# Performance work log

Measured on AMD Instinct MI355X. Metric: run time of the kernel, lower is better.

Reference implementation:

```python
import jax, jax.numpy as jnp
import numpy as np

N = 20000   # nodes
E = 160000  # edges
G = 32      # graphs in the batch
IN_DIM, HID, OUT = 27, 512, 256


def _linear_init(key, fan_in, fan_out):
    s = 1.0 / np.sqrt(fan_in)
    return jax.random.uniform(key, (fan_in, fan_out), jnp.float32, -s, s)


def setup_inputs() -> dict:
    key = jax.random.key(0)
    ks = jax.random.split(key, 16)
    feature = jax.random.normal(ks[0], (N, IN_DIM), jnp.float32)
    edge_src = jax.random.randint(ks[1], (E,), 0, N, jnp.int32)
    edge_dst = jax.random.randint(ks[2], (E,), 0, N, jnp.int32)
    graph_ids = jnp.sort(jax.random.randint(ks[3], (N,), 0, G, jnp.int32))
    dims = [(IN_DIM, HID), (HID, HID), (HID, OUT)]
    inp = {
        "feature": feature,
        "edge_src": edge_src,
        "edge_dst": edge_dst,
        "graph_ids": graph_ids,
    }
    k = 4
    for l, (fi, fo) in enumerate(dims):
        inp[f"W_self{l}"] = _linear_init(ks[k], fi, fo); k += 1
        inp[f"W_neigh{l}"] = _linear_init(ks[k], fi, fo); k += 1
        inp[f"b{l}"] = jnp.zeros((fo,), jnp.float32)
    return inp


def _sage_layer(h, edge_src, edge_dst, inv_deg, W_self, W_neigh, b):
    # mean aggregation of in-neighbors (src -> dst), DGL SAGEConv 'mean'
    msg = h[edge_src]                                   # [E, F]
    agg = jax.ops.segment_sum(msg, edge_dst, num_segments=N) * inv_deg  # [N, F]
    return h @ W_self + agg @ W_neigh + b


def reference(feature, edge_src, edge_dst, graph_ids,
              W_self0, W_neigh0, b0,
              W_self1, W_neigh1, b1,
              W_self2, W_neigh2, b2):
    ones_e = jnp.ones((E,), jnp.float32)
    deg = jax.ops.segment_sum(ones_e, edge_dst, num_segments=N)
    inv_deg = (1.0 / jnp.maximum(deg, 1.0))[:, None]    # [N, 1]

    h = _sage_layer(feature, edge_src, edge_dst, inv_deg, W_self0, W_neigh0, b0)
    h = jax.nn.relu(h)
    h = _sage_layer(h, edge_src, edge_dst, inv_deg, W_self1, W_neigh1, b1)
    h = jax.nn.relu(h)
    h = _sage_layer(h, edge_src, edge_dst, inv_deg, W_self2, W_neigh2, b2)
    # last layer: no activation (encoding=False -> last_activation=None)

    # AvgPooling: per-graph mean of node features
    ones_n = jnp.ones((N,), jnp.float32)
    counts = jax.ops.segment_sum(ones_n, graph_ids, num_segments=G)
    hg = jax.ops.segment_sum(h, graph_ids, num_segments=G) / jnp.maximum(counts, 1.0)[:, None]
    return h, hg
```

## Files before the change

### kernel.cpp

```cpp
#include <hip/hip_runtime.h>

constexpr int NN   = 20000;
constexpr int NE   = 160000;
constexpr int NG   = 32;
constexpr int IN   = 27;
constexpr int HID  = 512;
constexpr int OUT  = 256;
constexpr int MPAD = 20096;
constexpr int MT   = MPAD / 128;

typedef unsigned short u16;
typedef __bf16 bf16x8 __attribute__((ext_vector_type(8)));
typedef float  f32x4  __attribute__((ext_vector_type(4)));
typedef u16    u16x4  __attribute__((ext_vector_type(4)));

__device__ __forceinline__ u16 f2b(float x) {
  __bf16 h = (__bf16)x;
  return __builtin_bit_cast(u16, h);
}
__device__ __forceinline__ float b2f(u16 u) {
  __bf16 h = __builtin_bit_cast(__bf16, u);
  return (float)h;
}

#define GLOBAL_AS __attribute__((address_space(1)))
#define LDS_AS    __attribute__((address_space(3)))
__device__ __forceinline__ void gload_lds16(const void* g, void* l) {
  __builtin_amdgcn_global_load_lds((const GLOBAL_AS void*)g, (LDS_AS void*)l, 16, 0, 0);
}

__global__ void k_deg(const int* __restrict__ dst, int* __restrict__ deg) {
  int e = blockIdx.x * 256 + threadIdx.x;
  if (e < NE) atomicAdd(&deg[dst[e]], 1);
}

__global__ void k_scan(const int* __restrict__ deg, int* __restrict__ rowptr,
                       int* __restrict__ cursor, float* __restrict__ invdeg) {
  constexpr int CH = 20;
  __shared__ int wsum[16];
  const int tid = threadIdx.x;
  const int i0 = tid * CH;
  int loc[CH];
  int sum = 0;
#pragma unroll
  for (int j = 0; j < CH; ++j) {
    const int i = i0 + j;
    loc[j] = sum;
    sum += (i < NN) ? deg[i] : 0;
  }
  const int lane = tid & 63, wv = tid >> 6;
  int incl = sum;
#pragma unroll
  for (int off = 1; off < 64; off <<= 1) {
    int n = __shfl_up(incl, off);
    if (lane >= off) incl += n;
  }
  if (lane == 63) wsum[wv] = incl;
  __syncthreads();
  if (tid == 0) {
    int s = 0;
#pragma unroll
    for (int w = 0; w < 16; ++w) { int v = wsum[w]; wsum[w] = s + v; s += v; }
  }
  __syncthreads();
  const int wbase = (wv == 0) ? 0 : wsum[wv - 1];
  const int tbase = wbase + incl - sum;
#pragma unroll
  for (int j = 0; j < CH; ++j) {
    const int i = i0 + j;
    if (i < NN) {
      const int excl = tbase + loc[j];
      const int d = ((j + 1 < CH) ? loc[j + 1] : sum) - loc[j];
      rowptr[i] = excl;
      cursor[i] = excl;
      invdeg[i] = 1.0f / fmaxf((float)d, 1.0f);
    }
  }
  if (tid == 0) rowptr[NN] = wsum[15];
}

__global__ void k_scatter(const int* __restrict__ src, const int* __restrict__ dst,
                          int* __restrict__ cursor, int* __restrict__ ssrc) {
  int e = blockIdx.x * 256 + threadIdx.x;
  if (e < NE) {
    int p = atomicAdd(&cursor[dst[e]], 1);
    ssrc[p] = src[e];
  }
}

constexpr int WC0 = 512 * 64;
constexpr int WC1 = 512 * 1024;
constexpr int WC2 = 256 * 512;
constexpr int WCT = WC0 + WC1 + 2 * WC2;
__global__ void k_wconv_all(const float* __restrict__ Ws0, const float* __restrict__ Wn0,
                            const float* __restrict__ Ws1, const float* __restrict__ Wn1,
                            const float* __restrict__ Ws2, const float* __restrict__ Wn2,
                            u16* __restrict__ Bt0, u16* __restrict__ Bt1,
                            u16* __restrict__ BtS2, u16* __restrict__ BtN2) {
  int idx = blockIdx.x * 256 + threadIdx.x;
  if (idx < WC0) {
    const int n = idx / 64, k = idx % 64;
    float v = 0.0f;
    if (k < IN)           v = Ws0[(size_t)k * 512 + n];
    else if (k < 2 * IN)  v = Wn0[(size_t)(k - IN) * 512 + n];
    Bt0[idx] = f2b(v);
    return;
  }
  idx -= WC0;
  if (idx < WC1) {
    const int n = idx / 1024, k = idx % 1024;
    const float v = (k < 512) ? Ws1[(size_t)k * 512 + n] : Wn1[(size_t)(k - 512) * 512 + n];
    Bt1[idx] = f2b(v);
    return;
  }
  idx -= WC1;
  if (idx < WC2) {
    const int n = idx / 512, k = idx % 512;
    BtS2[idx] = f2b(Ws2[(size_t)k * 256 + n]);
    return;
  }
  idx -= WC2;
  if (idx < WC2) {
    const int n = idx / 512, k = idx % 512;
    BtN2[idx] = f2b(Wn2[(size_t)k * 256 + n]);
  }
}

__global__ void k_build_A0(const float* __restrict__ feat, const int* __restrict__ rowptr,
                           const int* __restrict__ ssrc, const float* __restrict__ invdeg,
                           u16* __restrict__ A0) {
  const int r = blockIdx.x, t = threadIdx.x;
  u16* row = A0 + (size_t)r * 64;
  if (r >= NN) { row[t] = 0; return; }
  if (t < IN) {
    row[t] = f2b(feat[(size_t)r * IN + t]);
    float s = 0.0f;
    const int e0 = rowptr[r], e1 = rowptr[r + 1];
    for (int e = e0; e < e1; ++e) s += feat[(size_t)ssrc[e] * IN + t];
    row[IN + t] = f2b(s * invdeg[r]);
  } else if (t >= 2 * IN) {
    row[t] = 0;
  }
}

__global__ void k_agg512(u16* __restrict__ A1, const int* __restrict__ rowptr,
                         const int* __restrict__ ssrc, const float* __restrict__ invdeg) {
  const int r = blockIdx.x, t = threadIdx.x;
  float a0 = 0, a1 = 0, a2 = 0, a3 = 0;
  const int e0 = rowptr[r], e1 = rowptr[r + 1];
  for (int e = e0; e < e1; ++e) {
    const u16x4 v = *(const u16x4*)(A1 + (size_t)ssrc[e] * 1024 + t * 4);
    a0 += b2f(v.x); a1 += b2f(v.y); a2 += b2f(v.z); a3 += b2f(v.w);
  }
  const float inv = invdeg[r];
  u16x4 o; o.x = f2b(a0 * inv); o.y = f2b(a1 * inv); o.z = f2b(a2 * inv); o.w = f2b(a3 * inv);
  *(u16x4*)(A1 + (size_t)r * 1024 + 512 + t * 4) = o;
}

__global__ void k_agg256(const u16* __restrict__ T2, const int* __restrict__ rowptr,
                         const int* __restrict__ ssrc, const float* __restrict__ invdeg,
                         float* __restrict__ AGG2) {
  const int r = blockIdx.x, t = threadIdx.x;
  float a0 = 0, a1 = 0, a2 = 0, a3 = 0;
  const int e0 = rowptr[r], e1 = rowptr[r + 1];
  for (int e = e0; e < e1; ++e) {
    const u16x4 v = *(const u16x4*)(T2 + (size_t)ssrc[e] * 256 + t * 4);
    a0 += b2f(v.x); a1 += b2f(v.y); a2 += b2f(v.z); a3 += b2f(v.w);
  }
  const float inv = invdeg[r];
  f32x4 o = {a0 * inv, a1 * inv, a2 * inv, a3 * inv};
  *(f32x4*)(AGG2 + (size_t)r * 256 + t * 4) = o;
}

__global__ __launch_bounds__(256) void k_gemm(
    const u16* __restrict__ A, int lda,
    const u16* __restrict__ Bt, int K,
    void* __restrict__ Out, int ldo,
    const float* __restrict__ bias,
    const float* __restrict__ addp,
    int flags) {
  __shared__ u16 As[128 * 64];
  __shared__ u16 Bs[128 * 64];
  const int tid = threadIdx.x;
  const int wid = tid >> 6, lane = tid & 63;
  const int l16 = lane & 15, lhi = lane >> 4;
  const int wr = wid >> 1, wc = wid & 1;
  const int row0 = blockIdx.x * 128, col0 = blockIdx.y * 128;

  const int tr    = tid >> 3;
  const int slot  = tid & 7;
  const int sslot = slot ^ (tr & 7);

  f32x4 acc[4][4] = {};

  for (int kt = 0; kt < K; kt += 64) {
#pragma unroll
    for (int i = 0; i < 4; ++i) {
      const int r = i * 32 + tr;
      gload_lds16(A  + (size_t)(row0 + r) * lda + kt + sslot * 8, &As[i * 2048 + wid * 512]);
      gload_lds16(Bt + (size_t)(col0 + r) * K   + kt + sslot * 8, &Bs[i * 2048 + wid * 512]);
    }
    __syncthreads();
#pragma unroll
    for (int ks = 0; ks < 2; ++ks) {
      bf16x8 af[4], bfr[4];
#pragma unroll
      for (int i = 0; i < 4; ++i) {
        const int r = wr * 64 + i * 16 + l16;
        const int s = (ks * 4 + lhi) ^ (r & 7);
        af[i] = *(const bf16x8*)&As[r * 64 + s * 8];
      }
#pragma unroll
      for (int n = 0; n < 4; ++n) {
        const int c = wc * 64 + n * 16 + l16;
        const int s = (ks * 4 + lhi) ^ (c & 7);
        bfr[n] = *(const bf16x8*)&Bs[c * 64 + s * 8];
      }
#pragma unroll
      for (int i = 0; i < 4; ++i)
#pragma unroll
        for (int n = 0; n < 4; ++n)
          acc[i][n] = __builtin_amdgcn_mfma_f32_16x16x32_bf16(af[i], bfr[n], acc[i][n], 0, 0, 0);
    }
    __syncthreads();
  }

  const bool relu = flags & 1;
  const bool f32o = flags & 2;
#pragma unroll
  for (int i = 0; i < 4; ++i) {
#pragma unroll
    for (int n = 0; n < 4; ++n) {
      const int C = col0 + wc * 64 + n * 16 + l16;
      const float bv = bias ? bias[C] : 0.0f;
#pragma unroll
      for (int q = 0; q < 4; ++q) {
        const int R = row0 + wr * 64 + i * 16 + lhi * 4 + q;
        float v = acc[i][n][q] + bv;
        if (f32o) {
          if (R < NN) {
            if (addp) v += addp[(size_t)R * ldo + C];
            ((float*)Out)[(size_t)R * ldo + C] = v;
          }
        } else {
          if (relu) v = fmaxf(v, 0.0f);
          ((u16*)Out)[(size_t)R * ldo + C] = f2b(v);
        }
      }
    }
  }
}

__device__ __forceinline__ int lower_bound_g(const int* __restrict__ gid, int g) {
  int lo = 0, hi = NN;
  while (lo < hi) {
    const int mid = (lo + hi) >> 1;
    if (gid[mid] < g) lo = mid + 1; else hi = mid;
  }
  return lo;
}
__global__ void k_pool(const float* __restrict__ h, const int* __restrict__ gid,
                       float* __restrict__ hg) {
  __shared__ int s_n0, s_n1;
  const int g = blockIdx.x >> 3, s = blockIdx.x & 7;
  const int t = threadIdx.x;
  if (t == 0) { s_n0 = lower_bound_g(gid, g); s_n1 = lower_bound_g(gid, g + 1); }
  __syncthreads();
  const int n0 = s_n0, n1 = s_n1;
  const int len = n1 - n0, chunk = (len + 7) / 8;
  const int a = n0 + s * chunk;
  const int b = min(a + chunk, n1);
  float acc = 0.0f;
  for (int i = a; i < b; ++i) acc += h[(size_t)i * 256 + t];
  if (b > a) atomicAdd(&hg[g * 256 + t], acc);
}
__global__ void k_pooldiv(float* __restrict__ hg, const int* __restrict__ gid) {
  __shared__ int s_c;
  const int g = blockIdx.x, t = threadIdx.x;
  if (t == 0) s_c = lower_bound_g(gid, g + 1) - lower_bound_g(gid, g);
  __syncthreads();
  hg[g * 256 + t] /= fmaxf((float)s_c, 1.0f);
}

constexpr size_t OFF_A0    = 0;
constexpr size_t OFF_A1    = OFF_A0   + (size_t)MPAD * 64  * 2;
constexpr size_t OFF_H1    = OFF_A1   + (size_t)MPAD * 1024 * 2;
constexpr size_t OFF_T2    = OFF_H1   + (size_t)MPAD * 512 * 2;
constexpr size_t OFF_AGG2  = OFF_T2   + (size_t)MPAD * 256 * 2;
constexpr size_t OFF_BT0   = OFF_AGG2 + (size_t)NN * 256 * 4;
constexpr size_t OFF_BT1   = OFF_BT0  + (size_t)512 * 64 * 2;
constexpr size_t OFF_BTS2  = OFF_BT1  + (size_t)512 * 1024 * 2;
constexpr size_t OFF_BTN2  = OFF_BTS2 + (size_t)256 * 512 * 2;
constexpr size_t OFF_DEG   = OFF_BTN2 + (size_t)256 * 512 * 2;
constexpr size_t OFF_RP    = OFF_DEG  + (size_t)NN * 4;
constexpr size_t OFF_CUR   = OFF_RP   + (size_t)(NN + 2) * 4;
constexpr size_t OFF_SSRC  = OFF_CUR  + (size_t)NN * 4;
constexpr size_t OFF_INVD  = OFF_SSRC + (size_t)NE * 4;

extern "C" void kernel_launch(void* const* d_in, const int* in_sizes, int n_in,
                              void* d_out, int out_size, void* d_ws, size_t ws_size,
                              hipStream_t stream) {
  const float* feature = (const float*)d_in[0];
  const int*   esrc    = (const int*)d_in[1];
  const int*   edst    = (const int*)d_in[2];
  const int*   gid     = (const int*)d_in[3];
  const float* Ws0 = (const float*)d_in[4],  *Wn0 = (const float*)d_in[5],  *b0 = (const float*)d_in[6];
  const float* Ws1 = (const float*)d_in[7],  *Wn1 = (const float*)d_in[8],  *b1 = (const float*)d_in[9];
  const float* Ws2 = (const float*)d_in[10], *Wn2 = (const float*)d_in[11], *b2 = (const float*)d_in[12];

  char* ws = (char*)d_ws;
  u16*   A0    = (u16*)  (ws + OFF_A0);
  u16*   A1    = (u16*)  (ws + OFF_A1);
  u16*   H1    = (u16*)  (ws + OFF_H1);
  u16*   T2    = (u16*)  (ws + OFF_T2);
  float* AGG2  = (float*)(ws + OFF_AGG2);
  u16*   Bt0   = (u16*)  (ws + OFF_BT0);
  u16*   Bt1   = (u16*)  (ws + OFF_BT1);
  u16*   BtS2  = (u16*)  (ws + OFF_BTS2);
  u16*   BtN2  = (u16*)  (ws + OFF_BTN2);
  int*   deg   = (int*)  (ws + OFF_DEG);
  int*   rp    = (int*)  (ws + OFF_RP);
  int*   cur   = (int*)  (ws + OFF_CUR);
  int*   ssrc  = (int*)  (ws + OFF_SSRC);
  float* invd  = (float*)(ws + OFF_INVD);

  float* out_h  = (float*)d_out;
  float* out_hg = out_h + (size_t)NN * OUT;

  hipMemsetAsync(deg,  0, (size_t)NN * 4, stream);
  hipMemsetAsync(out_hg, 0, (size_t)NG * OUT * 4, stream);

  k_deg    <<<(NE + 255) / 256, 256, 0, stream>>>(edst, deg);
  k_scan   <<<1, 1024, 0, stream>>>(deg, rp, cur, invd);
  k_scatter<<<(NE + 255) / 256, 256, 0, stream>>>(esrc, edst, cur, ssrc);

  k_wconv_all<<<(WCT + 255) / 256, 256, 0, stream>>>(Ws0, Wn0, Ws1, Wn1, Ws2, Wn2,
                                                     Bt0, Bt1, BtS2, BtN2);

  k_build_A0<<<MPAD, 64, 0, stream>>>(feature, rp, ssrc, invd, A0);
  k_gemm<<<dim3(MT, 4), 256, 0, stream>>>(A0, 64, Bt0, 64, A1, 1024, b0, nullptr, 1);

  k_agg512<<<NN, 128, 0, stream>>>(A1, rp, ssrc, invd);
  k_gemm<<<dim3(MT, 4), 256, 0, stream>>>(A1, 1024, Bt1, 1024, H1, 512, b1, nullptr, 1);

  k_gemm<<<dim3(MT, 2), 256, 0, stream>>>(H1, 512, BtN2, 512, T2, 256, nullptr, nullptr, 0);
  k_agg256<<<NN, 64, 0, stream>>>(T2, rp, ssrc, invd, AGG2);
  k_gemm<<<dim3(MT, 2), 256, 0, stream>>>(H1, 512, BtS2, 512, out_h, 256, b2, AGG2, 2);

  k_pool   <<<NG * 8, 256, 0, stream>>>(out_h, gid, out_hg);
  k_pooldiv<<<NG, 256, 0, stream>>>(out_hg, gid);
}
```

Baseline: 331.6 us.

## Aggregate layer-2 input before projection and fuse self/neighbor GEMM into one

The last layer now aggregates the 512-wide hidden features into a concatenated [H | agg(H)] buffer and runs a single K=1024 GEMM against stacked self/neighbor weights. This replaces the previous transform-then-aggregate order, which used two GEMMs, a 256-wide aggregation and an fp32 add pass. The cost is gathering 512-wide rows instead of 256-wide ones during aggregation. Pool division is also folded into the pool kernel, which drops one launch.

New measurement: 313.8 us. 5.4% less time.

```diff
diff --git a/kernel.cpp b/kernel.cpp
--- a/kernel.cpp
+++ b/kernel.cpp
@@ -90,13 +90,13 @@
 
 constexpr int WC0 = 512 * 64;
 constexpr int WC1 = 512 * 1024;
-constexpr int WC2 = 256 * 512;
-constexpr int WCT = WC0 + WC1 + 2 * WC2;
+constexpr int WC2 = 256 * 1024;
+constexpr int WCT = WC0 + WC1 + WC2;
 __global__ void k_wconv_all(const float* __restrict__ Ws0, const float* __restrict__ Wn0,
                             const float* __restrict__ Ws1, const float* __restrict__ Wn1,
                             const float* __restrict__ Ws2, const float* __restrict__ Wn2,
                             u16* __restrict__ Bt0, u16* __restrict__ Bt1,
-                            u16* __restrict__ BtS2, u16* __restrict__ BtN2) {
+                            u16* __restrict__ BtSN2) {
   int idx = blockIdx.x * 256 + threadIdx.x;
   if (idx < WC0) {
     const int n = idx / 64, k = idx % 64;
@@ -115,14 +115,9 @@
   }
   idx -= WC1;
   if (idx < WC2) {
-    const int n = idx / 512, k = idx % 512;
-    BtS2[idx] = f2b(Ws2[(size_t)k * 256 + n]);
-    return;
-  }
-  idx -= WC2;
-  if (idx < WC2) {
-    const int n = idx / 512, k = idx % 512;
-    BtN2[idx] = f2b(Wn2[(size_t)k * 256 + n]);
+    const int n = idx / 1024, k = idx % 1024;
+    const float v = (k < 512) ? Ws2[(size_t)k * 256 + n] : Wn2[(size_t)(k - 512) * 256 + n];
+    BtSN2[idx] = f2b(v);
   }
 }
 
@@ -143,33 +138,18 @@
   }
 }
 
-__global__ void k_agg512(u16* __restrict__ A1, const int* __restrict__ rowptr,
+__global__ void k_agg512(u16* __restrict__ X, const int* __restrict__ rowptr,
                          const int* __restrict__ ssrc, const float* __restrict__ invdeg) {
   const int r = blockIdx.x, t = threadIdx.x;
   float a0 = 0, a1 = 0, a2 = 0, a3 = 0;
   const int e0 = rowptr[r], e1 = rowptr[r + 1];
   for (int e = e0; e < e1; ++e) {
-    const u16x4 v = *(const u16x4*)(A1 + (size_t)ssrc[e] * 1024 + t * 4);
+    const u16x4 v = *(const u16x4*)(X + (size_t)ssrc[e] * 1024 + t * 4);
     a0 += b2f(v.x); a1 += b2f(v.y); a2 += b2f(v.z); a3 += b2f(v.w);
   }
   const float inv = invdeg[r];
   u16x4 o; o.x = f2b(a0 * inv); o.y = f2b(a1 * inv); o.z = f2b(a2 * inv); o.w = f2b(a3 * inv);
-  *(u16x4*)(A1 + (size_t)r * 1024 + 512 + t * 4) = o;
-}
-
-__global__ void k_agg256(const u16* __restrict__ T2, const int* __restrict__ rowptr,
-                         const int* __restrict__ ssrc, const float* __restrict__ invdeg,
-                         float* __restrict__ AGG2) {
-  const int r = blockIdx.x, t = threadIdx.x;
-  float a0 = 0, a1 = 0, a2 = 0, a3 = 0;
-  const int e0 = rowptr[r], e1 = rowptr[r + 1];
-  for (int e = e0; e < e1; ++e) {
-    const u16x4 v = *(const u16x4*)(T2 + (size_t)ssrc[e] * 256 + t * 4);
-    a0 += b2f(v.x); a1 += b2f(v.y); a2 += b2f(v.z); a3 += b2f(v.w);
-  }
-  const float inv = invdeg[r];
-  f32x4 o = {a0 * inv, a1 * inv, a2 * inv, a3 * inv};
-  *(f32x4*)(AGG2 + (size_t)r * 256 + t * 4) = o;
+  *(u16x4*)(X + (size_t)r * 1024 + 512 + t * 4) = o;
 }
 
 __global__ __launch_bounds__(256) void k_gemm(
@@ -177,7 +157,6 @@
     const u16* __restrict__ Bt, int K,
     void* __restrict__ Out, int ldo,
     const float* __restrict__ bias,
-    const float* __restrict__ addp,
     int flags) {
   __shared__ u16 As[128 * 64];
   __shared__ u16 Bs[128 * 64];
@@ -238,10 +217,7 @@
         const int R = row0 + wr * 64 + i * 16 + lhi * 4 + q;
         float v = acc[i][n][q] + bv;
         if (f32o) {
-          if (R < NN) {
-            if (addp) v += addp[(size_t)R * ldo + C];
-            ((float*)Out)[(size_t)R * ldo + C] = v;
-          }
+          if (R < NN) ((float*)Out)[(size_t)R * ldo + C] = v;
         } else {
           if (relu) v = fmaxf(v, 0.0f);
           ((u16*)Out)[(size_t)R * ldo + C] = f2b(v);
@@ -272,26 +248,19 @@
   const int b = min(a + chunk, n1);
   float acc = 0.0f;
   for (int i = a; i < b; ++i) acc += h[(size_t)i * 256 + t];
-  if (b > a) atomicAdd(&hg[g * 256 + t], acc);
-}
-__global__ void k_pooldiv(float* __restrict__ hg, const int* __restrict__ gid) {
-  __shared__ int s_c;
-  const int g = blockIdx.x, t = threadIdx.x;
-  if (t == 0) s_c = lower_bound_g(gid, g + 1) - lower_bound_g(gid, g);
-  __syncthreads();
-  hg[g * 256 + t] /= fmaxf((float)s_c, 1.0f);
+  if (b > a) {
+    const float inv = 1.0f / fmaxf((float)len, 1.0f);
+    atomicAdd(&hg[g * 256 + t], acc * inv);
+  }
 }
 
 constexpr size_t OFF_A0    = 0;
 constexpr size_t OFF_A1    = OFF_A0   + (size_t)MPAD * 64  * 2;
-constexpr size_t OFF_H1    = OFF_A1   + (size_t)MPAD * 1024 * 2;
-constexpr size_t OFF_T2    = OFF_H1   + (size_t)MPAD * 512 * 2;
-constexpr size_t OFF_AGG2  = OFF_T2   + (size_t)MPAD * 256 * 2;
-constexpr size_t OFF_BT0   = OFF_AGG2 + (size_t)NN * 256 * 4;
+constexpr size_t OFF_A2    = OFF_A1   + (size_t)MPAD * 1024 * 2;
+constexpr size_t OFF_BT0   = OFF_A2   + (size_t)MPAD * 1024 * 2;
 constexpr size_t OFF_BT1   = OFF_BT0  + (size_t)512 * 64 * 2;
-constexpr size_t OFF_BTS2  = OFF_BT1  + (size_t)512 * 1024 * 2;
-constexpr size_t OFF_BTN2  = OFF_BTS2 + (size_t)256 * 512 * 2;
-constexpr size_t OFF_DEG   = OFF_BTN2 + (size_t)256 * 512 * 2;
+constexpr size_t OFF_BTSN2 = OFF_BT1  + (size_t)512 * 1024 * 2;
+constexpr size_t OFF_DEG   = OFF_BTSN2+ (size_t)256 * 1024 * 2;
 constexpr size_t OFF_RP    = OFF_DEG  + (size_t)NN * 4;
 constexpr size_t OFF_CUR   = OFF_RP   + (size_t)(NN + 2) * 4;
 constexpr size_t OFF_SSRC  = OFF_CUR  + (size_t)NN * 4;
@@ -311,13 +280,10 @@
   char* ws = (char*)d_ws;
   u16*   A0    = (u16*)  (ws + OFF_A0);
   u16*   A1    = (u16*)  (ws + OFF_A1);
-  u16*   H1    = (u16*)  (ws + OFF_H1);
-  u16*   T2    = (u16*)  (ws + OFF_T2);
-  float* AGG2  = (float*)(ws + OFF_AGG2);
+  u16*   A2    = (u16*)  (ws + OFF_A2);
   u16*   Bt0   = (u16*)  (ws + OFF_BT0);
   u16*   Bt1   = (u16*)  (ws + OFF_BT1);
-  u16*   BtS2  = (u16*)  (ws + OFF_BTS2);
-  u16*   BtN2  = (u16*)  (ws + OFF_BTN2);
+  u16*   BtSN2 = (u16*)  (ws + OFF_BTSN2);
   int*   deg   = (int*)  (ws + OFF_DEG);
   int*   rp    = (int*)  (ws + OFF_RP);
   int*   cur   = (int*)  (ws + OFF_CUR);
@@ -335,18 +301,16 @@
   k_scatter<<<(NE + 255) / 256, 256, 0, stream>>>(esrc, edst, cur, ssrc);
 
   k_wconv_all<<<(WCT + 255) / 256, 256, 0, stream>>>(Ws0, Wn0, Ws1, Wn1, Ws2, Wn2,
-                                                     Bt0, Bt1, BtS2, BtN2);
+                                                     Bt0, Bt1, BtSN2);
 
   k_build_A0<<<MPAD, 64, 0, stream>>>(feature, rp, ssrc, invd, A0);
-  k_gemm<<<dim3(MT, 4), 256, 0, stream>>>(A0, 64, Bt0, 64, A1, 1024, b0, nullptr, 1);
+  k_gemm<<<dim3(MT, 4), 256, 0, stream>>>(A0, 64, Bt0, 64, A1, 1024, b0, 1);
 
   k_agg512<<<NN, 128, 0, stream>>>(A1, rp, ssrc, invd);
-  k_gemm<<<dim3(MT, 4), 256, 0, stream>>>(A1, 1024, Bt1, 1024, H1, 512, b1, nullptr, 1);
-
-  k_gemm<<<dim3(MT, 2), 256, 0, stream>>>(H1, 512, BtN2, 512, T2, 256, nullptr, nullptr, 0);
-  k_agg256<<<NN, 64, 0, stream>>>(T2, rp, ssrc, invd, AGG2);
-  k_gemm<<<dim3(MT, 2), 256, 0, stream>>>(H1, 512, BtS2, 512, out_h, 256, b2, AGG2, 2);
-
-  k_pool   <<<NG * 8, 256, 0, stream>>>(out_h, gid, out_hg);
-  k_pooldiv<<<NG, 256, 0, stream>>>(out_hg, gid);
-}
+  k_gemm<<<dim3(MT, 4), 256, 0, stream>>>(A1, 1024, Bt1, 1024, A2, 1024, b1, 1);
+
+  k_agg512<<<NN, 128, 0, stream>>>(A2, rp, ssrc, invd);
+  k_gemm<<<dim3(MT, 2), 256, 0, stream>>>(A2, 1024, BtSN2, 1024, out_h, 256, b2, 2);
+
+  k_pool<<<NG * 8, 256, 0, stream>>>(out_h, gid, out_hg);
+}
```
